# Kernel tuning notes

Hardware: AMD Instinct MI355X
Metric: run time of the kernel (lower is better)

The kernel has to match this reference:

```python
import jax, jax.numpy as jnp
import numpy as np

B, Z, H, T = 4096, 512, 384, 32


def setup_inputs() -> dict:
    key = jax.random.key(0)
    ks = jax.random.split(key, 8)
    z = jax.random.normal(ks[0], (B, Z), dtype=jnp.float32)
    h_init = jax.random.normal(ks[1], (B, H), dtype=jnp.float32) * 0.01
    s1 = 1.0 / np.sqrt(Z)
    s23 = 1.0 / np.sqrt(2 * H)
    W1 = jax.random.uniform(ks[2], (H, Z), jnp.float32, -s1, s1)
    b1 = jax.random.uniform(ks[3], (H,), jnp.float32, -s1, s1)
    W2 = jax.random.uniform(ks[4], (Z, 2 * H), jnp.float32, -s23, s23)
    b2 = jax.random.uniform(ks[5], (Z,), jnp.float32, -s23, s23)
    W3 = jax.random.uniform(ks[6], (H, 2 * H), jnp.float32, -s23, s23)
    b3 = jax.random.uniform(ks[7], (H,), jnp.float32, -s23, s23)
    return {"z": z, "h_init": h_init, "W1": W1, "b1": b1, "W2": W2,
            "b2": b2, "W3": W3, "b3": b3, "n_frames": T}


def reference(z, h_init, W1, b1, W2, b2, W3, b3, n_frames):
    # training path: r = w_residual*4 / n_frames (const decay)
    r = jnp.asarray(0.2 * 4.0 / n_frames, dtype=z.dtype)
    lrelu = lambda x: jax.nn.leaky_relu(x, 0.01)

    def step(carry, _):
        zp, hp = carry
        temp = jnp.concatenate([lrelu(zp @ W1.T + b1), hp], axis=-1)  # [B, 2H]
        zn = lrelu(temp @ W2.T + b2) * r + zp
        hn = lrelu(temp @ W3.T + b3) * r + hp
        return (zn, hn), zn

    _, outs = jax.lax.scan(step, (z, h_init), None, length=n_frames - 1)
    all_out = jnp.concatenate([z[None], outs], axis=0)        # [T, B, Z]
    out = (all_out - z[None]).transpose(1, 0, 2)               # [B, T, Z]
    return out.reshape(-1, z.shape[-1])                        # [B*T, Z]
```

## Files before the change

kernel.cpp:

```cpp
#include <hip/hip_runtime.h>
#include <hip/hip_bf16.h>


typedef __bf16 bf16x8 __attribute__((ext_vector_type(8)));
typedef float f32x4 __attribute__((ext_vector_type(4)));

#define B_ROWS 4096
#define ZDIM 512
#define HDIM 384
#define TFRAMES 32

__device__ __forceinline__ void load16(const void* g, void* s) {
    __builtin_amdgcn_global_load_lds(
        (const __attribute__((address_space(1))) void*)g,
        (__attribute__((address_space(3))) void*)s, 16, 0, 0);
}

__device__ __forceinline__ float lrelu(float x) { return x >= 0.f ? x : 0.01f * x; }

__global__ __launch_bounds__(256) void k1_gemm(
    const __hip_bfloat16* __restrict__ A,
    const __hip_bfloat16* __restrict__ W,
    const float* __restrict__ bias,
    __hip_bfloat16* __restrict__ T)
{
    constexpr int BM = 64, BN = 128, BK = 64, K = 512, LDA = 512, LDW = 512, LDT = 768;
    __shared__ __hip_bfloat16 As[BM * BK];
    __shared__ __hip_bfloat16 Bs[BN * BK];
    const int tid = threadIdx.x;
    const int w = tid >> 6, l = tid & 63;
    const int wm = w >> 1, wn = w & 1;
    const int m0 = blockIdx.y * BM, n0 = blockIdx.x * BN;
    const int lrow = l >> 3, lcol = (l & 7) * 8;

    f32x4 acc[2][4] = {};

    for (int kb = 0; kb < K; kb += BK) {
        __syncthreads();
        #pragma unroll
        for (int i = 0; i < BM / 32; ++i) {
            int p = w * (BM / 32) + i;
            int rr = p * 8 + lrow;
            load16(A + (size_t)(m0 + rr) * LDA + kb + lcol, As + rr * BK + lcol);
        }
        #pragma unroll
        for (int i = 0; i < BN / 32; ++i) {
            int p = w * (BN / 32) + i;
            int rr = p * 8 + lrow;
            load16(W + (size_t)(n0 + rr) * LDW + kb + lcol, Bs + rr * BK + lcol);
        }
        __builtin_amdgcn_s_waitcnt(0);
        __syncthreads();
        #pragma unroll
        for (int ks = 0; ks < BK; ks += 32) {
            bf16x8 af[2], bfr[4];
            #pragma unroll
            for (int i = 0; i < 2; ++i)
                af[i] = *(const bf16x8*)(const void*)(As + (wm * 32 + i * 16 + (l & 15)) * BK + ks + (l >> 4) * 8);
            #pragma unroll
            for (int j = 0; j < 4; ++j)
                bfr[j] = *(const bf16x8*)(const void*)(Bs + (wn * 64 + j * 16 + (l & 15)) * BK + ks + (l >> 4) * 8);
            #pragma unroll
            for (int i = 0; i < 2; ++i)
                #pragma unroll
                for (int j = 0; j < 4; ++j)
                    acc[i][j] = __builtin_amdgcn_mfma_f32_16x16x32_bf16(af[i], bfr[j], acc[i][j], 0, 0, 0);
        }
    }
    #pragma unroll
    for (int j = 0; j < 4; ++j) {
        int col = n0 + wn * 64 + j * 16 + (l & 15);
        float bv = bias[col];
        #pragma unroll
        for (int i = 0; i < 2; ++i) {
            int rbase = m0 + wm * 32 + i * 16 + (l >> 4) * 4;
            #pragma unroll
            for (int rg = 0; rg < 4; ++rg) {
                float v = lrelu(acc[i][j][rg] + bv);
                T[(size_t)(rbase + rg) * LDT + col] = __float2bfloat16(v);
            }
        }
    }
}

__global__ __launch_bounds__(256) void k2_gemm(
    const __hip_bfloat16* __restrict__ A,
    const __hip_bfloat16* __restrict__ W2b,
    const __hip_bfloat16* __restrict__ W3b,
    const float* __restrict__ b2, const float* __restrict__ b3,
    float* __restrict__ zs, float* __restrict__ hs,
    __hip_bfloat16* __restrict__ zb, __hip_bfloat16* __restrict__ tnext,
    const float* __restrict__ z0, float* __restrict__ out, int t)
{
    constexpr int BM = 128, BN = 128, BK = 64, K = 768, LDA = 768, LDW = 768;
    __shared__ __hip_bfloat16 As[BM * BK];
    __shared__ __hip_bfloat16 Bs[BN * BK];
    const int tid = threadIdx.x;
    const int w = tid >> 6, l = tid & 63;
    const int wm = w >> 1, wn = w & 1;
    const int m0 = blockIdx.y * BM, n0 = blockIdx.x * BN;
    const bool isZ = (n0 < ZDIM);
    const __hip_bfloat16* W = isZ ? (W2b + (size_t)n0 * LDW) : (W3b + (size_t)(n0 - ZDIM) * LDW);
    const int lrow = l >> 3, lcol = (l & 7) * 8;

    f32x4 acc[4][4] = {};

    for (int kb = 0; kb < K; kb += BK) {
        __syncthreads();
        #pragma unroll
        for (int i = 0; i < 4; ++i) {
            int p = w * 4 + i;
            int rr = p * 8 + lrow;
            load16(A + (size_t)(m0 + rr) * LDA + kb + lcol, As + rr * BK + lcol);
        }
        #pragma unroll
        for (int i = 0; i < 4; ++i) {
            int p = w * 4 + i;
            int rr = p * 8 + lrow;
            load16(W + (size_t)rr * LDW + kb + lcol, Bs + rr * BK + lcol);
        }
        __builtin_amdgcn_s_waitcnt(0);
        __syncthreads();
        #pragma unroll
        for (int ks = 0; ks < BK; ks += 32) {
            bf16x8 af[4], bfr[4];
            #pragma unroll
            for (int i = 0; i < 4; ++i)
                af[i] = *(const bf16x8*)(const void*)(As + (wm * 64 + i * 16 + (l & 15)) * BK + ks + (l >> 4) * 8);
            #pragma unroll
            for (int j = 0; j < 4; ++j)
                bfr[j] = *(const bf16x8*)(const void*)(Bs + (wn * 64 + j * 16 + (l & 15)) * BK + ks + (l >> 4) * 8);
            #pragma unroll
            for (int i = 0; i < 4; ++i)
                #pragma unroll
                for (int j = 0; j < 4; ++j)
                    acc[i][j] = __builtin_amdgcn_mfma_f32_16x16x32_bf16(af[i], bfr[j], acc[i][j], 0, 0, 0);
        }
    }

    const float rdecay = (float)(0.2 * 4.0 / 32.0);
    #pragma unroll
    for (int j = 0; j < 4; ++j) {
        int col = n0 + wn * 64 + j * 16 + (l & 15);
        float bv = isZ ? b2[col] : b3[col - ZDIM];
        #pragma unroll
        for (int i = 0; i < 4; ++i) {
            int rbase = m0 + wm * 64 + i * 16 + (l >> 4) * 4;
            #pragma unroll
            for (int rg = 0; rg < 4; ++rg) {
                int row = rbase + rg;
                float v = lrelu(acc[i][j][rg] + bv) * rdecay;
                if (isZ) {
                    size_t idx = (size_t)row * ZDIM + col;
                    float zn = v + zs[idx];
                    zs[idx] = zn;
                    zb[idx] = __float2bfloat16(zn);
                    out[((size_t)row * TFRAMES + t) * ZDIM + col] = zn - z0[idx];
                } else {
                    int c2 = col - ZDIM;
                    size_t idx = (size_t)row * HDIM + c2;
                    float hn = v + hs[idx];
                    hs[idx] = hn;
                    tnext[(size_t)row * 768 + HDIM + c2] = __float2bfloat16(hn);
                }
            }
        }
    }
}

__global__ void cvt_kernel(const float* __restrict__ s, __hip_bfloat16* __restrict__ d, int n) {
    for (int i = blockIdx.x * blockDim.x + threadIdx.x; i < n; i += gridDim.x * blockDim.x)
        d[i] = __float2bfloat16(s[i]);
}

__global__ void h_to_temp_kernel(const float* __restrict__ h, __hip_bfloat16* __restrict__ temp, int n) {
    for (int i = blockIdx.x * blockDim.x + threadIdx.x; i < n; i += gridDim.x * blockDim.x) {
        int b = i / HDIM, j = i - b * HDIM;
        temp[(size_t)b * 768 + HDIM + j] = __float2bfloat16(h[i]);
    }
}

__global__ void zero_out0_kernel(float* __restrict__ out) {
    int n = B_ROWS * ZDIM;
    for (int i = blockIdx.x * blockDim.x + threadIdx.x; i < n; i += gridDim.x * blockDim.x) {
        int b = i >> 9, j = i & 511;
        out[(size_t)b * TFRAMES * ZDIM + j] = 0.f;
    }
}

extern "C" void kernel_launch(void* const* d_in, const int* in_sizes, int n_in,
                              void* d_out, int out_size, void* d_ws, size_t ws_size,
                              hipStream_t stream) {
    const float* z  = (const float*)d_in[0];
    const float* h0 = (const float*)d_in[1];
    const float* W1 = (const float*)d_in[2];
    const float* b1 = (const float*)d_in[3];
    const float* W2 = (const float*)d_in[4];
    const float* b2 = (const float*)d_in[5];
    const float* W3 = (const float*)d_in[6];
    const float* b3 = (const float*)d_in[7];
    float* out = (float*)d_out;

    char* p = (char*)d_ws;
    float* zs = (float*)p;              p += (size_t)B_ROWS * ZDIM * 4;
    float* hs = (float*)p;              p += (size_t)B_ROWS * HDIM * 4;
    __hip_bfloat16* zb    = (__hip_bfloat16*)p; p += (size_t)B_ROWS * ZDIM * 2;
    __hip_bfloat16* temp0 = (__hip_bfloat16*)p; p += (size_t)B_ROWS * 768 * 2;
    __hip_bfloat16* temp1 = (__hip_bfloat16*)p; p += (size_t)B_ROWS * 768 * 2;
    __hip_bfloat16* W1b   = (__hip_bfloat16*)p; p += (size_t)HDIM * ZDIM * 2;
    __hip_bfloat16* W2b   = (__hip_bfloat16*)p; p += (size_t)ZDIM * 768 * 2;
    __hip_bfloat16* W3b   = (__hip_bfloat16*)p; p += (size_t)HDIM * 768 * 2;

    hipMemcpyAsync(zs, z,  (size_t)B_ROWS * ZDIM * 4, hipMemcpyDeviceToDevice, stream);
    hipMemcpyAsync(hs, h0, (size_t)B_ROWS * HDIM * 4, hipMemcpyDeviceToDevice, stream);
    cvt_kernel<<<256, 256, 0, stream>>>(z, zb, B_ROWS * ZDIM);
    h_to_temp_kernel<<<256, 256, 0, stream>>>(h0, temp1, B_ROWS * HDIM);
    cvt_kernel<<<64, 256, 0, stream>>>(W1, W1b, HDIM * ZDIM);
    cvt_kernel<<<128, 256, 0, stream>>>(W2, W2b, ZDIM * 768);
    cvt_kernel<<<96, 256, 0, stream>>>(W3, W3b, HDIM * 768);
    zero_out0_kernel<<<256, 256, 0, stream>>>(out);

    for (int t = 1; t < TFRAMES; ++t) {
        __hip_bfloat16* tcur  = (t & 1) ? temp1 : temp0;
        __hip_bfloat16* tnext = (t & 1) ? temp0 : temp1;
        k1_gemm<<<dim3(HDIM / 128, B_ROWS / 64), 256, 0, stream>>>(zb, W1b, b1, tcur);
        k2_gemm<<<dim3((ZDIM + HDIM) / 128, B_ROWS / 128), 256, 0, stream>>>(
            tcur, W2b, W3b, b2, b3, zs, hs, zb, tnext, z, out, t);
    }
}
```

Before: 2.006 ms.

## Fuse all timesteps into one persistent kernel with LDS-resident state

Replaces the per-timestep pair of GEMM launches with a single kernel where each block owns 32 batch rows and iterates all frames, keeping z (fp32) and h/temp (fp16) in shared memory. Weights are converted to fp16 and read directly from global memory by each wave without LDS staging. This removes launch overhead and global round-trips of intermediate state, at the cost of only 128 blocks and repeated per-block weight reads from L2; h is now stored in fp16, changing precision.

```diff
diff --git a/kernel.cpp b/kernel.cpp
--- a/kernel.cpp
+++ b/kernel.cpp
@@ -1,190 +1,179 @@
 #include <hip/hip_runtime.h>
-#include <hip/hip_bf16.h>
-
-
-typedef __bf16 bf16x8 __attribute__((ext_vector_type(8)));
+#include <type_traits>
+
+
+typedef _Float16 f16;
+typedef f16 f16x8 __attribute__((ext_vector_type(8)));
 typedef float f32x4 __attribute__((ext_vector_type(4)));
-
-#define B_ROWS 4096
-#define ZDIM 512
-#define HDIM 384
-#define TFRAMES 32
-
-__device__ __forceinline__ void load16(const void* g, void* s) {
-    __builtin_amdgcn_global_load_lds(
-        (const __attribute__((address_space(1))) void*)g,
-        (__attribute__((address_space(3))) void*)s, 16, 0, 0);
+typedef float f32x16 __attribute__((ext_vector_type(16)));
+
+#define ZD 512
+#define HD 384
+#define TT 32
+#define BM 32
+#define LZ 516
+#define LT 392
+
+__device__ __forceinline__ float lrelu(float x) { return x >= 0.f ? x : 0.01f * x; }
+
+__global__ void cvt_f32_f16(const float* __restrict__ s, f16* __restrict__ d, int n) {
+    for (int i = blockIdx.x * blockDim.x + threadIdx.x; i < n; i += gridDim.x * blockDim.x)
+        d[i] = (f16)s[i];
 }
 
-__device__ __forceinline__ float lrelu(float x) { return x >= 0.f ? x : 0.01f * x; }
-
-__global__ __launch_bounds__(256) void k1_gemm(
-    const __hip_bfloat16* __restrict__ A,
-    const __hip_bfloat16* __restrict__ W,
-    const float* __restrict__ bias,
-    __hip_bfloat16* __restrict__ T)
+__global__ __launch_bounds__(512) void latrec(
+    const float* __restrict__ z0g, const float* __restrict__ h0g,
+    const f16* __restrict__ W1h, const f16* __restrict__ W2h, const f16* __restrict__ W3h,
+    const float* __restrict__ b1g, const float* __restrict__ b2g, const float* __restrict__ b3g,
+    float* __restrict__ out)
 {
-    constexpr int BM = 64, BN = 128, BK = 64, K = 512, LDA = 512, LDW = 512, LDT = 768;
-    __shared__ __hip_bfloat16 As[BM * BK];
-    __shared__ __hip_bfloat16 Bs[BN * BK];
+    __shared__ float zf[BM * LZ];
+    __shared__ f16 tz[BM * LT];
+    __shared__ f16 hb[2][BM * LT];
+    __shared__ float bias[1280];
+
     const int tid = threadIdx.x;
     const int w = tid >> 6, l = tid & 63;
-    const int wm = w >> 1, wn = w & 1;
-    const int m0 = blockIdx.y * BM, n0 = blockIdx.x * BN;
-    const int lrow = l >> 3, lcol = (l & 7) * 8;
-
-    f32x4 acc[2][4] = {};
-
-    for (int kb = 0; kb < K; kb += BK) {
+    const int lm = l & 31;
+    const int lk = (l >> 5) * 8;
+    const int m0 = blockIdx.x * BM;
+
+    for (int i = tid; i < HD; i += 512) bias[i] = b1g[i];
+    for (int i = tid; i < ZD; i += 512) bias[384 + i] = b2g[i];
+    for (int i = tid; i < HD; i += 512) bias[896 + i] = b3g[i];
+    for (int i = tid; i < BM * 128; i += 512) {
+        int r = i >> 7, c = (i & 127) << 2;
+        f32x4 v = *(const f32x4*)(z0g + (size_t)(m0 + r) * ZD + c);
+        *(f32x4*)(zf + r * LZ + c) = v;
+        f32x4 zr = {0.f, 0.f, 0.f, 0.f};
+        __builtin_nontemporal_store(zr.x, out + ((size_t)(m0 + r) * TT) * ZD + c);
+        __builtin_nontemporal_store(zr.y, out + ((size_t)(m0 + r) * TT) * ZD + c + 1);
+        __builtin_nontemporal_store(zr.z, out + ((size_t)(m0 + r) * TT) * ZD + c + 2);
+        __builtin_nontemporal_store(zr.w, out + ((size_t)(m0 + r) * TT) * ZD + c + 3);
+    }
+    for (int i = tid; i < BM * HD; i += 512) {
+        int r = i / HD, c = i - r * HD;
+        hb[0][r * LT + c] = (f16)h0g[(size_t)(m0 + r) * HD + c];
+    }
+    __syncthreads();
+
+    for (int t = 1; t < TT; ++t) {
+        const f16* hcur = hb[(t - 1) & 1];
+        f16* hnxt = hb[t & 1];
+
+        {
+            const int nt0 = (w < 4) ? 2 * w : (w + 4);
+            const int nt1 = (w < 4) ? 2 * w + 1 : nt0;
+            const float* ap = zf + lm * LZ + lk;
+            const f16* wp0 = W1h + (size_t)(nt0 * 32 + lm) * ZD + lk;
+            const f16* wp1 = W1h + (size_t)(nt1 * 32 + lm) * ZD + lk;
+            auto run1 = [&](auto NTC) {
+                constexpr int NT = decltype(NTC)::value;
+                f32x16 a0 = {}, a1 = {};
+                #pragma unroll 4
+                for (int ks = 0; ks < ZD; ks += 16) {
+                    f32x4 x0 = *(const f32x4*)(ap + ks);
+                    f32x4 x1 = *(const f32x4*)(ap + ks + 4);
+                    f16x8 af;
+                    #pragma unroll
+                    for (int e = 0; e < 4; ++e) { af[e] = (f16)x0[e]; af[4 + e] = (f16)x1[e]; }
+                    f16x8 bf0 = *(const f16x8*)(wp0 + ks);
+                    a0 = __builtin_amdgcn_mfma_f32_32x32x16_f16(af, bf0, a0, 0, 0, 0);
+                    if constexpr (NT == 2) {
+                        f16x8 bf1 = *(const f16x8*)(wp1 + ks);
+                        a1 = __builtin_amdgcn_mfma_f32_32x32x16_f16(af, bf1, a1, 0, 0, 0);
+                    }
+                }
+                {
+                    int c = nt0 * 32 + lm; float bv = bias[c];
+                    #pragma unroll
+                    for (int rg = 0; rg < 16; ++rg) {
+                        int row = (rg & 3) + 8 * (rg >> 2) + 4 * (l >> 5);
+                        tz[row * LT + c] = (f16)lrelu(a0[rg] + bv);
+                    }
+                }
+                if constexpr (NT == 2) {
+                    int c = nt1 * 32 + lm; float bv = bias[c];
+                    #pragma unroll
+                    for (int rg = 0; rg < 16; ++rg) {
+                        int row = (rg & 3) + 8 * (rg >> 2) + 4 * (l >> 5);
+                        tz[row * LT + c] = (f16)lrelu(a1[rg] + bv);
+                    }
+                }
+            };
+            if (w < 4) run1(std::integral_constant<int, 2>{});
+            else       run1(std::integral_constant<int, 1>{});
+        }
         __syncthreads();
-        #pragma unroll
-        for (int i = 0; i < BM / 32; ++i) {
-            int p = w * (BM / 32) + i;
-            int rr = p * 8 + lrow;
-            load16(A + (size_t)(m0 + rr) * LDA + kb + lcol, As + rr * BK + lcol);
+
+        {
+            const int t0 = w, t1 = w + 8;
+            const int t2 = (w < 4) ? 16 + 2 * w : 20 + w;
+            const int t3 = (w < 4) ? 17 + 2 * w : t2;
+            auto wptr = [&](int nt) {
+                return (nt < 16) ? W2h + (size_t)(nt * 32 + lm) * 768 + lk
+                                 : W3h + (size_t)((nt - 16) * 32 + lm) * 768 + lk;
+            };
+            const f16* wp0 = wptr(t0); const f16* wp1 = wptr(t1);
+            const f16* wp2 = wptr(t2); const f16* wp3 = wptr(t3);
+            const f16* ap1 = tz + lm * LT + lk;
+            const f16* ap2 = hcur + lm * LT + lk;
+
+            auto epi2 = [&](const f32x16& ac, int nt) {
+                if (nt < 16) {
+                    int c = nt * 32 + lm;
+                    float bv = bias[384 + c];
+                    #pragma unroll
+                    for (int rg = 0; rg < 16; ++rg) {
+                        int row = (rg & 3) + 8 * (rg >> 2) + 4 * (l >> 5);
+                        float v = lrelu(ac[rg] + bv) * 0.025f;
+                        float zn = zf[row * LZ + c] + v;
+                        zf[row * LZ + c] = zn;
+                        size_t gr = (size_t)(m0 + row);
+                        float o = zn - z0g[gr * ZD + c];
+                        __builtin_nontemporal_store(o, out + (gr * TT + t) * ZD + c);
+                    }
+                } else {
+                    int c = (nt - 16) * 32 + lm;
+                    float bv = bias[896 + c];
+                    #pragma unroll
+                    for (int rg = 0; rg < 16; ++rg) {
+                        int row = (rg & 3) + 8 * (rg >> 2) + 4 * (l >> 5);
+                        float v = lrelu(ac[rg] + bv) * 0.025f;
+                        float hn = (float)hcur[row * LT + c] + v;
+                        hnxt[row * LT + c] = (f16)hn;
+                    }
+                }
+            };
+
+            auto run2 = [&](auto NTC) {
+                constexpr int NT = decltype(NTC)::value;
+                f32x16 a0 = {}, a1 = {}, a2 = {}, a3 = {};
+                auto khalf = [&](const f16* ab, int kw) {
+                    #pragma unroll 4
+                    for (int ks = 0; ks < HD; ks += 16) {
+                        f16x8 af = *(const f16x8*)(ab + ks);
+                        f16x8 b0 = *(const f16x8*)(wp0 + kw + ks);
+                        a0 = __builtin_amdgcn_mfma_f32_32x32x16_f16(af, b0, a0, 0, 0, 0);
+                        f16x8 b1 = *(const f16x8*)(wp1 + kw + ks);
+                        a1 = __builtin_amdgcn_mfma_f32_32x32x16_f16(af, b1, a1, 0, 0, 0);
+                        f16x8 b2 = *(const f16x8*)(wp2 + kw + ks);
+                        a2 = __builtin_amdgcn_mfma_f32_32x32x16_f16(af, b2, a2, 0, 0, 0);
+                        if constexpr (NT == 4) {
+                            f16x8 b3 = *(const f16x8*)(wp3 + kw + ks);
+                            a3 = __builtin_amdgcn_mfma_f32_32x32x16_f16(af, b3, a3, 0, 0, 0);
+                        }
+                    }
+                };
+                khalf(ap1, 0);
+                khalf(ap2, HD);
+                epi2(a0, t0); epi2(a1, t1); epi2(a2, t2);
+                if constexpr (NT == 4) epi2(a3, t3);
+            };
+            if (w < 4) run2(std::integral_constant<int, 4>{});
+            else       run2(std::integral_constant<int, 3>{});
         }
-        #pragma unroll
-        for (int i = 0; i < BN / 32; ++i) {
-            int p = w * (BN / 32) + i;
-            int rr = p * 8 + lrow;
-            load16(W + (size_t)(n0 + rr) * LDW + kb + lcol, Bs + rr * BK + lcol);
-        }
-        __builtin_amdgcn_s_waitcnt(0);
         __syncthreads();
-        #pragma unroll
-        for (int ks = 0; ks < BK; ks += 32) {
-            bf16x8 af[2], bfr[4];
-            #pragma unroll
-            for (int i = 0; i < 2; ++i)
-                af[i] = *(const bf16x8*)(const void*)(As + (wm * 32 + i * 16 + (l & 15)) * BK + ks + (l >> 4) * 8);
-            #pragma unroll
-            for (int j = 0; j < 4; ++j)
-                bfr[j] = *(const bf16x8*)(const void*)(Bs + (wn * 64 + j * 16 + (l & 15)) * BK + ks + (l >> 4) * 8);
-            #pragma unroll
-            for (int i = 0; i < 2; ++i)
-                #pragma unroll
-                for (int j = 0; j < 4; ++j)
-                    acc[i][j] = __builtin_amdgcn_mfma_f32_16x16x32_bf16(af[i], bfr[j], acc[i][j], 0, 0, 0);
-        }
-    }
-    #pragma unroll
-    for (int j = 0; j < 4; ++j) {
-        int col = n0 + wn * 64 + j * 16 + (l & 15);
-        float bv = bias[col];
-        #pragma unroll
-        for (int i = 0; i < 2; ++i) {
-            int rbase = m0 + wm * 32 + i * 16 + (l >> 4) * 4;
-            #pragma unroll
-            for (int rg = 0; rg < 4; ++rg) {
-                float v = lrelu(acc[i][j][rg] + bv);
-                T[(size_t)(rbase + rg) * LDT + col] = __float2bfloat16(v);
-            }
-        }
-    }
-}
-
-__global__ __launch_bounds__(256) void k2_gemm(
-    const __hip_bfloat16* __restrict__ A,
-    const __hip_bfloat16* __restrict__ W2b,
-    const __hip_bfloat16* __restrict__ W3b,
-    const float* __restrict__ b2, const float* __restrict__ b3,
-    float* __restrict__ zs, float* __restrict__ hs,
-    __hip_bfloat16* __restrict__ zb, __hip_bfloat16* __restrict__ tnext,
-    const float* __restrict__ z0, float* __restrict__ out, int t)
-{
-    constexpr int BM = 128, BN = 128, BK = 64, K = 768, LDA = 768, LDW = 768;
-    __shared__ __hip_bfloat16 As[BM * BK];
-    __shared__ __hip_bfloat16 Bs[BN * BK];
-    const int tid = threadIdx.x;
-    const int w = tid >> 6, l = tid & 63;
-    const int wm = w >> 1, wn = w & 1;
-    const int m0 = blockIdx.y * BM, n0 = blockIdx.x * BN;
-    const bool isZ = (n0 < ZDIM);
-    const __hip_bfloat16* W = isZ ? (W2b + (size_t)n0 * LDW) : (W3b + (size_t)(n0 - ZDIM) * LDW);
-    const int lrow = l >> 3, lcol = (l & 7) * 8;
-
-    f32x4 acc[4][4] = {};
-
-    for (int kb = 0; kb < K; kb += BK) {
-        __syncthreads();
-        #pragma unroll
-        for (int i = 0; i < 4; ++i) {
-            int p = w * 4 + i;
-            int rr = p * 8 + lrow;
-            load16(A + (size_t)(m0 + rr) * LDA + kb + lcol, As + rr * BK + lcol);
-        }
-        #pragma unroll
-        for (int i = 0; i < 4; ++i) {
-            int p = w * 4 + i;
-            int rr = p * 8 + lrow;
-            load16(W + (size_t)rr * LDW + kb + lcol, Bs + rr * BK + lcol);
-        }
-        __builtin_amdgcn_s_waitcnt(0);
-        __syncthreads();
-        #pragma unroll
-        for (int ks = 0; ks < BK; ks += 32) {
-            bf16x8 af[4], bfr[4];
-            #pragma unroll
-            for (int i = 0; i < 4; ++i)
-                af[i] = *(const bf16x8*)(const void*)(As + (wm * 64 + i * 16 + (l & 15)) * BK + ks + (l >> 4) * 8);
-            #pragma unroll
-            for (int j = 0; j < 4; ++j)
-                bfr[j] = *(const bf16x8*)(const void*)(Bs + (wn * 64 + j * 16 + (l & 15)) * BK + ks + (l >> 4) * 8);
-            #pragma unroll
-            for (int i = 0; i < 4; ++i)
-                #pragma unroll
-                for (int j = 0; j < 4; ++j)
-                    acc[i][j] = __builtin_amdgcn_mfma_f32_16x16x32_bf16(af[i], bfr[j], acc[i][j], 0, 0, 0);
-        }
-    }
-
-    const float rdecay = (float)(0.2 * 4.0 / 32.0);
-    #pragma unroll
-    for (int j = 0; j < 4; ++j) {
-        int col = n0 + wn * 64 + j * 16 + (l & 15);
-        float bv = isZ ? b2[col] : b3[col - ZDIM];
-        #pragma unroll
-        for (int i = 0; i < 4; ++i) {
-            int rbase = m0 + wm * 64 + i * 16 + (l >> 4) * 4;
-            #pragma unroll
-            for (int rg = 0; rg < 4; ++rg) {
-                int row = rbase + rg;
-                float v = lrelu(acc[i][j][rg] + bv) * rdecay;
-                if (isZ) {
-                    size_t idx = (size_t)row * ZDIM + col;
-                    float zn = v + zs[idx];
-                    zs[idx] = zn;
-                    zb[idx] = __float2bfloat16(zn);
-                    out[((size_t)row * TFRAMES + t) * ZDIM + col] = zn - z0[idx];
-                } else {
-                    int c2 = col - ZDIM;
-                    size_t idx = (size_t)row * HDIM + c2;
-                    float hn = v + hs[idx];
-                    hs[idx] = hn;
-                    tnext[(size_t)row * 768 + HDIM + c2] = __float2bfloat16(hn);
-                }
-            }
-        }
-    }
-}
-
-__global__ void cvt_kernel(const float* __restrict__ s, __hip_bfloat16* __restrict__ d, int n) {
-    for (int i = blockIdx.x * blockDim.x + threadIdx.x; i < n; i += gridDim.x * blockDim.x)
-        d[i] = __float2bfloat16(s[i]);
-}
-
-__global__ void h_to_temp_kernel(const float* __restrict__ h, __hip_bfloat16* __restrict__ temp, int n) {
-    for (int i = blockIdx.x * blockDim.x + threadIdx.x; i < n; i += gridDim.x * blockDim.x) {
-        int b = i / HDIM, j = i - b * HDIM;
-        temp[(size_t)b * 768 + HDIM + j] = __float2bfloat16(h[i]);
-    }
-}
-
-__global__ void zero_out0_kernel(float* __restrict__ out) {
-    int n = B_ROWS * ZDIM;
-    for (int i = blockIdx.x * blockDim.x + threadIdx.x; i < n; i += gridDim.x * blockDim.x) {
-        int b = i >> 9, j = i & 511;
-        out[(size_t)b * TFRAMES * ZDIM + j] = 0.f;
     }
 }
 
@@ -202,29 +191,13 @@
     float* out = (float*)d_out;
 
     char* p = (char*)d_ws;
-    float* zs = (float*)p;              p += (size_t)B_ROWS * ZDIM * 4;
-    float* hs = (float*)p;              p += (size_t)B_ROWS * HDIM * 4;
-    __hip_bfloat16* zb    = (__hip_bfloat16*)p; p += (size_t)B_ROWS * ZDIM * 2;
-    __hip_bfloat16* temp0 = (__hip_bfloat16*)p; p += (size_t)B_ROWS * 768 * 2;
-    __hip_bfloat16* temp1 = (__hip_bfloat16*)p; p += (size_t)B_ROWS * 768 * 2;
-    __hip_bfloat16* W1b   = (__hip_bfloat16*)p; p += (size_t)HDIM * ZDIM * 2;
-    __hip_bfloat16* W2b   = (__hip_bfloat16*)p; p += (size_t)ZDIM * 768 * 2;
-    __hip_bfloat16* W3b   = (__hip_bfloat16*)p; p += (size_t)HDIM * 768 * 2;
-
-    hipMemcpyAsync(zs, z,  (size_t)B_ROWS * ZDIM * 4, hipMemcpyDeviceToDevice, stream);
-    hipMemcpyAsync(hs, h0, (size_t)B_ROWS * HDIM * 4, hipMemcpyDeviceToDevice, stream);
-    cvt_kernel<<<256, 256, 0, stream>>>(z, zb, B_ROWS * ZDIM);
-    h_to_temp_kernel<<<256, 256, 0, stream>>>(h0, temp1, B_ROWS * HDIM);
-    cvt_kernel<<<64, 256, 0, stream>>>(W1, W1b, HDIM * ZDIM);
-    cvt_kernel<<<128, 256, 0, stream>>>(W2, W2b, ZDIM * 768);
-    cvt_kernel<<<96, 256, 0, stream>>>(W3, W3b, HDIM * 768);
-    zero_out0_kernel<<<256, 256, 0, stream>>>(out);
-
-    for (int t = 1; t < TFRAMES; ++t) {
-        __hip_bfloat16* tcur  = (t & 1) ? temp1 : temp0;
-        __hip_bfloat16* tnext = (t & 1) ? temp0 : temp1;
-        k1_gemm<<<dim3(HDIM / 128, B_ROWS / 64), 256, 0, stream>>>(zb, W1b, b1, tcur);
-        k2_gemm<<<dim3((ZDIM + HDIM) / 128, B_ROWS / 128), 256, 0, stream>>>(
-            tcur, W2b, W3b, b2, b3, zs, hs, zb, tnext, z, out, t);
-    }
+    f16* W1h = (f16*)p; p += (size_t)HD * ZD * 2;
+    f16* W2h = (f16*)p; p += (size_t)ZD * 768 * 2;
+    f16* W3h = (f16*)p; p += (size_t)HD * 768 * 2;
+
+    cvt_f32_f16<<<96, 256, 0, stream>>>(W1, W1h, HD * ZD);
+    cvt_f32_f16<<<192, 256, 0, stream>>>(W2, W2h, ZD * 768);
+    cvt_f32_f16<<<144, 256, 0, stream>>>(W3, W3h, HD * 768);
+
+    latrec<<<4096 / BM, 512, 0, stream>>>(z, h0, W1h, W2h, W3h, b1, b2, b3, out);
 }
```

After: 1.843 ms. 8.1% less time.
